# Optimization experiments

Measured on AMD Instinct MI355X. Metric: run time of the kernel, lower is better.

The kernel has to match this reference:

```python
import jax, jax.numpy as jnp
import numpy as np

D_MODEL = 512
N_HEADS = 8
MAX_CH = 128
LN_EPS = 1e-5


def setup_inputs() -> dict:
    key = jax.random.key(0)
    ks = jax.random.split(key, 8)
    B, T, C, D = 8, 256, 64, D_MODEL
    x = jax.random.normal(ks[0], (B, T, C, D), dtype=jnp.float32)
    # nn.MultiheadAttention params: packed in_proj [3D, D], out_proj [D, D]
    in_proj_w = jax.random.normal(ks[1], (3 * D, D), dtype=jnp.float32) * 0.02
    in_proj_b = jnp.zeros((3 * D,), dtype=jnp.float32)
    out_proj_w = jax.random.normal(ks[2], (D, D), dtype=jnp.float32) * 0.02
    out_proj_b = jnp.zeros((D,), dtype=jnp.float32)
    ln_g = jnp.ones((D,), dtype=jnp.float32)
    ln_b = jnp.zeros((D,), dtype=jnp.float32)
    rel_pos_bias = jax.random.normal(ks[3], (N_HEADS, MAX_CH, MAX_CH), dtype=jnp.float32) * 0.02
    return {"x": x, "in_proj_w": in_proj_w, "in_proj_b": in_proj_b,
            "out_proj_w": out_proj_w, "out_proj_b": out_proj_b,
            "ln_g": ln_g, "ln_b": ln_b, "rel_pos_bias": rel_pos_bias}


def _layernorm(x, g, b):
    mu = jnp.mean(x, axis=-1, keepdims=True)
    var = jnp.var(x, axis=-1, keepdims=True)
    return (x - mu) * jax.lax.rsqrt(var + LN_EPS) * g + b


def reference(x, in_proj_w, in_proj_b, out_proj_w, out_proj_b, ln_g, ln_b, rel_pos_bias):
    B, T, C, D = x.shape
    H = N_HEADS
    hd = D // H
    N = B * T
    xf = x.reshape(N, C, D)
    # 2D additive attn_mask: mean over heads of rel-pos bias, broadcast over heads/batch
    bias = jnp.mean(rel_pos_bias[:, :C, :C], axis=0)  # [C, C]
    qkv = xf @ in_proj_w.T + in_proj_b  # [N, C, 3D]
    q, k, v = jnp.split(qkv, 3, axis=-1)
    q = q.reshape(N, C, H, hd)
    k = k.reshape(N, C, H, hd)
    v = v.reshape(N, C, H, hd)
    scores = jnp.einsum('nqhd,nkhd->nhqk', q, k) / jnp.sqrt(jnp.float32(hd))
    scores = scores + bias[None, None, :, :]
    attn = jax.nn.softmax(scores, axis=-1)
    ctx = jnp.einsum('nhqk,nkhd->nqhd', attn, v).reshape(N, C, D)
    attn_out = ctx @ out_proj_w.T + out_proj_b
    out = _layernorm(xf + attn_out, ln_g, ln_b)
    return out.reshape(B, T, C, D)
```

## Files before the change

### kernel.cpp

```cpp
#include <hip/hip_runtime.h>
#include <stdint.h>
#include <stddef.h>


typedef __attribute__((ext_vector_type(8))) short short8;
typedef __attribute__((ext_vector_type(4))) float f32x4;

typedef __attribute__((address_space(3))) unsigned int as3_u32;
typedef __attribute__((address_space(1))) unsigned int as1_u32;

#define VMCNT5 asm volatile("s_waitcnt vmcnt(5)" ::: "memory")
#define VMCNT4 asm volatile("s_waitcnt vmcnt(4)" ::: "memory")
#define VMCNT0 asm volatile("s_waitcnt vmcnt(0)" ::: "memory")
#define LGKM0  asm volatile("s_waitcnt lgkmcnt(0)" ::: "memory")
#define BARR() __builtin_amdgcn_s_barrier()
#define PRIO1  __builtin_amdgcn_s_setprio(1)
#define PRIO0  __builtin_amdgcn_s_setprio(0)

__device__ __forceinline__ unsigned short f2bf(float f) {
  unsigned u = __builtin_bit_cast(unsigned, f);
  u = (u + 0x7FFFu + ((u >> 16) & 1u)) >> 16;
  return (unsigned short)u;
}

__device__ __forceinline__ f32x4 mfma16(short8 a, short8 b, f32x4 c) {
  return __builtin_amdgcn_mfma_f32_16x16x32_bf16(a, b, c, 0, 0, 0);
}

__device__ __forceinline__ short8 rd72(const char* buf, int row, int kelem) {
  return *(const short8*)(buf + row * 144 + kelem * 2);
}

__device__ __forceinline__ void stage16k(char* ldsbase, const char* gsrc, int w, int lane) {
#pragma unroll
  for (int j = 0; j < 4; ++j) {
    int off = j * 4096 + w * 1024;
    __builtin_amdgcn_global_load_lds((const as1_u32*)(gsrc + off + lane * 16),
                                     (as3_u32*)(ldsbase + off), 16, 0, 0);
  }
}

__global__ void prep_kernel(const float* __restrict__ wqkv_f,
                            const float* __restrict__ wo_f,
                            const float* __restrict__ rel,
                            unsigned short* __restrict__ wt,
                            float* __restrict__ bias2d) {
  int b = blockIdx.x, tid = threadIdx.x;
  if (b < 128) {
    unsigned short* dst = wt + (size_t)b * 8192;
#pragma unroll
    for (int t = 0; t < 4; ++t) {
      int u = t * 256 + tid;
      int row = u >> 4, us = u & 15;
      int kg = (us & 8) | ((us ^ row) & 7);
      const float* src;
      if (b < 96) {
        int h = b / 12, i = b % 12;
        int rg = i >> 2, kc = i & 3;
        src = wqkv_f + (size_t)(rg * 512 + h * 64 + row) * 512 + kc * 128 + kg * 8;
      } else {
        int cw = b - 96;
        int kc = cw >> 3, ng = cw & 7;
        src = wo_f + (size_t)(ng * 64 + row) * 512 + kc * 128 + kg * 8;
      }
      float4 a = *(const float4*)src;
      float4 c = *(const float4*)(src + 4);
      unsigned p0 = (unsigned)f2bf(a.x) | ((unsigned)f2bf(a.y) << 16);
      unsigned p1 = (unsigned)f2bf(a.z) | ((unsigned)f2bf(a.w) << 16);
      unsigned p2 = (unsigned)f2bf(c.x) | ((unsigned)f2bf(c.y) << 16);
      unsigned p3 = (unsigned)f2bf(c.z) | ((unsigned)f2bf(c.w) << 16);
      *(uint4*)(dst + u * 8) = make_uint4(p0, p1, p2, p3);
    }
  } else {
    int idx = (b - 128) * 256 + tid;
    int m = idx >> 6, nn = idx & 63;
    float s = 0.f;
#pragma unroll
    for (int hh = 0; hh < 8; ++hh) s += rel[hh * 16384 + m * 128 + nn];
    bias2d[idx] = s * 0.125f;
  }
}

__global__ __launch_bounds__(256, 2) void attn_qkv(
    const float* __restrict__ x,
    const char* __restrict__ wq,
    const float* __restrict__ bqkv,
    const float* __restrict__ bias2d,
    char* __restrict__ ctxg) {
  __shared__ __attribute__((aligned(16))) char smem[60416];
  char* B0 = smem;
  char* B1 = smem + 9216;
  char* B2 = smem + 18432;
  char* WSb = smem + 27648;

  const int n = blockIdx.x;
  const int tid = threadIdx.x;
  const int w = tid >> 6, lane = tid & 63;
  const int l15 = lane & 15, g = lane >> 4;
  const int wm = w >> 1, wn = w & 1;
  const int mrow = w * 16 + g * 4;
  const int wrow = w * 16 + l15;

  float b2d[16];
#pragma unroll
  for (int nt = 0; nt < 4; ++nt)
#pragma unroll
    for (int r = 0; r < 4; ++r)
      b2d[nt * 4 + r] = bias2d[(mrow + r) * 64 + nt * 16 + l15];

  stage16k(WSb, wq, w, lane);

  short8 xf[32];
#pragma unroll
  for (int mt = 0; mt < 2; ++mt) {
    const float* xr = x + ((size_t)n * 64 + wm * 32 + mt * 16 + l15) * 512;
#pragma unroll
    for (int kk = 0; kk < 16; ++kk) {
      float4 a = *(const float4*)(xr + kk * 32 + g * 8);
      float4 c = *(const float4*)(xr + kk * 32 + g * 8 + 4);
      short8 s;
      s[0] = (short)f2bf(a.x); s[1] = (short)f2bf(a.y);
      s[2] = (short)f2bf(a.z); s[3] = (short)f2bf(a.w);
      s[4] = (short)f2bf(c.x); s[5] = (short)f2bf(c.y);
      s[6] = (short)f2bf(c.z); s[7] = (short)f2bf(c.w);
      xf[mt * 16 + kk] = s;
    }
  }

  int b = 0;
  for (int h = 0; h < 8; ++h) {
    float bq2[2], bk2[2], bv2[2];
#pragma unroll
    for (int nt = 0; nt < 2; ++nt) {
      int col = h * 64 + wn * 32 + nt * 16 + l15;
      bq2[nt] = bqkv[col];
      bk2[nt] = bqkv[512 + col];
      bv2[nt] = bqkv[1024 + col];
    }
#pragma unroll
    for (int rg = 0; rg < 3; ++rg) {
      f32x4 acc[2][2] = {};
#pragma unroll
      for (int c = 0; c < 4; ++c) {
        if (b < 95)
          stage16k(WSb + (((b + 1) & 1) << 14), wq + (size_t)(b + 1) * 16384, w, lane);
        if (b < 95) { VMCNT4; } else { VMCNT0; }
        BARR();
        const char* ws = WSb + ((b & 1) << 14);
        PRIO1;
#pragma unroll
        for (int ks = 0; ks < 4; ++ks) {
#pragma unroll
          for (int nt = 0; nt < 2; ++nt) {
            int row = wn * 32 + nt * 16 + l15;
            int kg = ks * 4 + g;
            int us = (kg & 8) | ((kg ^ row) & 7);
            short8 bfr = *(const short8*)(ws + row * 256 + us * 16);
            acc[0][nt] = mfma16(xf[c * 4 + ks], bfr, acc[0][nt]);
            acc[1][nt] = mfma16(xf[16 + c * 4 + ks], bfr, acc[1][nt]);
          }
        }
        PRIO0;
        LGKM0; BARR();
        ++b;
      }
      if (rg == 0) {
#pragma unroll
        for (int mt = 0; mt < 2; ++mt)
#pragma unroll
          for (int nt = 0; nt < 2; ++nt)
#pragma unroll
            for (int r = 0; r < 4; ++r)
              *(unsigned short*)(B0 + (wm * 32 + mt * 16 + g * 4 + r) * 144 +
                                 (wn * 32 + nt * 16 + l15) * 2) =
                  f2bf(acc[mt][nt][r] + bq2[nt]);
      } else if (rg == 1) {
#pragma unroll
        for (int mt = 0; mt < 2; ++mt)
#pragma unroll
          for (int nt = 0; nt < 2; ++nt)
#pragma unroll
            for (int r = 0; r < 4; ++r)
              *(unsigned short*)(B1 + (wm * 32 + mt * 16 + g * 4 + r) * 144 +
                                 (wn * 32 + nt * 16 + l15) * 2) =
                  f2bf(acc[mt][nt][r] + bk2[nt]);
      } else {
#pragma unroll
        for (int mt = 0; mt < 2; ++mt)
#pragma unroll
          for (int nt = 0; nt < 2; ++nt) {
            unsigned short p0 = f2bf(acc[mt][nt][0] + bv2[nt]);
            unsigned short p1 = f2bf(acc[mt][nt][1] + bv2[nt]);
            unsigned short p2 = f2bf(acc[mt][nt][2] + bv2[nt]);
            unsigned short p3 = f2bf(acc[mt][nt][3] + bv2[nt]);
            unsigned lo = (unsigned)p0 | ((unsigned)p1 << 16);
            unsigned hi = (unsigned)p2 | ((unsigned)p3 << 16);
            *(uint2*)(B2 + (wn * 32 + nt * 16 + l15) * 144 +
                      (wm * 32 + mt * 16 + g * 4) * 2) = make_uint2(lo, hi);
          }
      }
    }
    LGKM0; BARR();

    {
      f32x4 sc[4] = {};
      short8 aq0 = rd72(B0, wrow, g * 8);
      short8 aq1 = rd72(B0, wrow, 32 + g * 8);
#pragma unroll
      for (int nt = 0; nt < 4; ++nt)
        sc[nt] = mfma16(aq0, rd72(B1, nt * 16 + l15, g * 8), sc[nt]);
#pragma unroll
      for (int nt = 0; nt < 4; ++nt)
        sc[nt] = mfma16(aq1, rd72(B1, nt * 16 + l15, 32 + g * 8), sc[nt]);
      float mx[4] = {-1e30f, -1e30f, -1e30f, -1e30f};
#pragma unroll
      for (int nt = 0; nt < 4; ++nt)
#pragma unroll
        for (int r = 0; r < 4; ++r) {
          float v = sc[nt][r] * 0.125f + b2d[nt * 4 + r];
          sc[nt][r] = v;
          mx[r] = fmaxf(mx[r], v);
        }
#pragma unroll
      for (int mk = 1; mk < 16; mk <<= 1)
#pragma unroll
        for (int r = 0; r < 4; ++r) mx[r] = fmaxf(mx[r], __shfl_xor(mx[r], mk));
      float sm[4] = {0.f, 0.f, 0.f, 0.f};
#pragma unroll
      for (int nt = 0; nt < 4; ++nt)
#pragma unroll
        for (int r = 0; r < 4; ++r) {
          float e = __expf(sc[nt][r] - mx[r]);
          sc[nt][r] = e;
          sm[r] += e;
        }
#pragma unroll
      for (int mk = 1; mk < 16; mk <<= 1)
#pragma unroll
        for (int r = 0; r < 4; ++r) sm[r] += __shfl_xor(sm[r], mk);
      float inv[4];
#pragma unroll
      for (int r = 0; r < 4; ++r) inv[r] = 1.0f / sm[r];
#pragma unroll
      for (int nt = 0; nt < 4; ++nt)
#pragma unroll
        for (int r = 0; r < 4; ++r)
          *(unsigned short*)(B0 + (mrow + r) * 144 + (nt * 16 + l15) * 2) =
              f2bf(sc[nt][r] * inv[r]);
    }

    f32x4 cv[4] = {};
    {
      short8 ap0 = rd72(B0, wrow, g * 8);
      short8 ap1 = rd72(B0, wrow, 32 + g * 8);
#pragma unroll
      for (int nt = 0; nt < 4; ++nt)
        cv[nt] = mfma16(ap0, rd72(B2, nt * 16 + l15, g * 8), cv[nt]);
#pragma unroll
      for (int nt = 0; nt < 4; ++nt)
        cv[nt] = mfma16(ap1, rd72(B2, nt * 16 + l15, 32 + g * 8), cv[nt]);
    }
    LGKM0; BARR();
#pragma unroll
    for (int nt = 0; nt < 4; ++nt)
#pragma unroll
      for (int r = 0; r < 4; ++r)
        *(unsigned short*)(B2 + (mrow + r) * 144 + (nt * 16 + l15) * 2) =
            f2bf(cv[nt][r]);
    LGKM0; BARR();

    {
      char* cdst = ctxg + (size_t)n * 131072 + (h >> 1) * 16384 + (h & 1) * 128;
#pragma unroll
      for (int it = 0; it < 2; ++it) {
        int flat = it * 256 + tid;
        int row = flat >> 3, uu = flat & 7;
        uint4 v = *(const uint4*)(B2 + row * 144 + uu * 16);
        int slot = uu ^ (row & 7);
        *(uint4*)(cdst + row * 256 + slot * 16) = v;
      }
    }
  }
}

__global__ __launch_bounds__(256, 2) void oproj_ln(
    const char* __restrict__ ctxg,
    const char* __restrict__ wo,
    const float* __restrict__ bo,
    const float* __restrict__ x,
    const float* __restrict__ lng,
    const float* __restrict__ lnb,
    float* __restrict__ out) {
  __shared__ __attribute__((aligned(16))) char smem[65536];
  char* WB = smem;
  char* CB = smem + 32768;
  float* EP  = (float*)smem;
  float* SM1 = (float*)(smem + 32768);
  float* SM2 = (float*)(smem + 33408);

  const int n = blockIdx.x;
  const int tid = threadIdx.x;
  const int w = tid >> 6, lane = tid & 63;
  const int l15 = lane & 15, g = lane >> 4;
  const int um = w >> 1, un = w & 1;

  const char* cbase = ctxg + (size_t)n * 131072;

  stage16k(CB, cbase, w, lane);
  stage16k(WB, wo, w, lane);

  f32x4 acc[8][2][2] = {};

  for (int kc = 0; kc < 4; ++kc) {
    short8 actx[2][4];
#pragma unroll
    for (int ng = 0; ng < 8; ++ng) {
      int b = kc * 8 + ng;
      if (b < 31)
        stage16k(WB + (((b + 1) & 1) << 14), wo + (size_t)(b + 1) * 16384, w, lane);
      if ((ng & 1) == 0 && kc < 3) {
        int p = ng >> 1;
        int off = p * 4096 + w * 1024;
        __builtin_amdgcn_global_load_lds(
            (const as1_u32*)(cbase + (kc + 1) * 16384 + off + lane * 16),
            (as3_u32*)(CB + (((kc + 1) & 1) << 14) + off), 16, 0, 0);
      }
      if (b < 31) { VMCNT5; } else { VMCNT0; }
      BARR();
      const char* cb = CB + ((kc & 1) << 14);
      if (ng == 0) {
#pragma unroll
        for (int mt = 0; mt < 2; ++mt)
#pragma unroll
          for (int ks = 0; ks < 4; ++ks) {
            int row = um * 32 + mt * 16 + l15;
            int u = ks * 4 + g;
            int us = u ^ (row & 7);
            actx[mt][ks] = *(const short8*)(cb + row * 256 + us * 16);
          }
      }
      const char* ws = WB + ((b & 1) << 14);
      PRIO1;
#pragma unroll
      for (int ks = 0; ks < 4; ++ks) {
#pragma unroll
        for (int nt = 0; nt < 2; ++nt) {
          int row = un * 32 + nt * 16 + l15;
          int kg = ks * 4 + g;
          int us = (kg & 8) | ((kg ^ row) & 7);
          short8 bfr = *(const short8*)(ws + row * 256 + us * 16);
          acc[ng][0][nt] = mfma16(actx[0][ks], bfr, acc[ng][0][nt]);
          acc[ng][1][nt] = mfma16(actx[1][ks], bfr, acc[ng][1][nt]);
        }
      }
      PRIO0;
      LGKM0; BARR();
    }
  }

  VMCNT0;
  const float* xblk = x + (size_t)n * 32768;
  float* oblk = out + (size_t)n * 32768;
  float s1[2][4] = {}, s2[2][4] = {};

#pragma unroll
  for (int ng = 0; ng < 8; ++ng) {
#pragma unroll
    for (int t = 0; t < 4; ++t) {
      int flat = t * 256 + tid;
      int row = flat >> 4, f4 = flat & 15;
      float4 v = *(const float4*)(xblk + row * 512 + ng * 64 + f4 * 4);
      *(float4*)(EP + row * 68 + f4 * 4) = v;
    }
    LGKM0; BARR();
    float boA[2];
#pragma unroll
    for (int nt = 0; nt < 2; ++nt) boA[nt] = bo[ng * 64 + un * 32 + nt * 16 + l15];
#pragma unroll
    for (int mt = 0; mt < 2; ++mt)
#pragma unroll
      for (int nt = 0; nt < 2; ++nt)
#pragma unroll
        for (int r = 0; r < 4; ++r) {
          int row = um * 32 + mt * 16 + g * 4 + r;
          float xv = EP[row * 68 + un * 32 + nt * 16 + l15];
          float v = acc[ng][mt][nt][r] + boA[nt] + xv;
          acc[ng][mt][nt][r] = v;
          s1[mt][r] += v;
          s2[mt][r] += v * v;
        }
    LGKM0; BARR();
  }
#pragma unroll
  for (int mk = 1; mk < 16; mk <<= 1)
#pragma unroll
    for (int mt = 0; mt < 2; ++mt)
#pragma unroll
      for (int r = 0; r < 4; ++r) {
        s1[mt][r] += __shfl_xor(s1[mt][r], mk);
        s2[mt][r] += __shfl_xor(s2[mt][r], mk);
      }
  if (l15 == 0) {
#pragma unroll
    for (int mt = 0; mt < 2; ++mt)
#pragma unroll
      for (int r = 0; r < 4; ++r) {
        int row = um * 32 + mt * 16 + g * 4 + r;
        SM1[row * 2 + un] = s1[mt][r];
        SM2[row * 2 + un] = s2[mt][r];
      }
  }
  LGKM0; BARR();
  float mu[2][4], rs[2][4];
#pragma unroll
  for (int mt = 0; mt < 2; ++mt)
#pragma unroll
    for (int r = 0; r < 4; ++r) {
      int row = um * 32 + mt * 16 + g * 4 + r;
      float a1 = SM1[row * 2] + SM1[row * 2 + 1];
      float a2 = SM2[row * 2] + SM2[row * 2 + 1];
      float m = a1 * (1.0f / 512.0f);
      float var = a2 * (1.0f / 512.0f) - m * m;
      mu[mt][r] = m;
      rs[mt][r] = rsqrtf(var + 1e-5f);
    }
  BARR();
#pragma unroll
  for (int ng = 0; ng < 8; ++ng) {
    float lgA[2], lbA[2];
#pragma unroll
    for (int nt = 0; nt < 2; ++nt) {
      int col = ng * 64 + un * 32 + nt * 16 + l15;
      lgA[nt] = lng[col];
      lbA[nt] = lnb[col];
    }
#pragma unroll
    for (int mt = 0; mt < 2; ++mt)
#pragma unroll
      for (int nt = 0; nt < 2; ++nt)
#pragma unroll
        for (int r = 0; r < 4; ++r) {
          int row = um * 32 + mt * 16 + g * 4 + r;
          EP[row * 68 + un * 32 + nt * 16 + l15] =
              (acc[ng][mt][nt][r] - mu[mt][r]) * rs[mt][r] * lgA[nt] + lbA[nt];
        }
    LGKM0; BARR();
#pragma unroll
    for (int t = 0; t < 4; ++t) {
      int flat = t * 256 + tid;
      int row = flat >> 4, f4 = flat & 15;
      *(float4*)(oblk + row * 512 + ng * 64 + f4 * 4) =
          *(const float4*)(EP + row * 68 + f4 * 4);
    }
    BARR();
  }
}

extern "C" void kernel_launch(void* const* d_in, const int* in_sizes, int n_in,
                              void* d_out, int out_size, void* d_ws, size_t ws_size,
                              hipStream_t stream) {
  const float* x    = (const float*)d_in[0];
  const float* wqkv = (const float*)d_in[1];
  const float* bqkv = (const float*)d_in[2];
  const float* wo   = (const float*)d_in[3];
  const float* bo   = (const float*)d_in[4];
  const float* lng  = (const float*)d_in[5];
  const float* lnb  = (const float*)d_in[6];
  const float* rel  = (const float*)d_in[7];

  unsigned short* wt = (unsigned short*)d_ws;
  float* bias2d = (float*)((char*)d_ws + 128 * 16384);
  const char* wqc = (const char*)d_ws;
  const char* woc = (const char*)d_ws + 96 * 16384;

  prep_kernel<<<144, 256, 0, stream>>>(wqkv, wo, rel, wt, bias2d);
  attn_qkv<<<2048, 256, 0, stream>>>(x, wqc, bqkv, bias2d, (char*)d_out);
  oproj_ln<<<2048, 256, 0, stream>>>((const char*)d_out, woc, bo, x, lng, lnb,
                                     (float*)d_out);
}
```

Baseline: 578.2 us.

## Triple-buffer QKV weight staging and switch attention tiles to XOR-swizzled layout

```diff
diff --git a/kernel.cpp b/kernel.cpp
--- a/kernel.cpp
+++ b/kernel.cpp
@@ -9,6 +9,7 @@
 typedef __attribute__((address_space(3))) unsigned int as3_u32;
 typedef __attribute__((address_space(1))) unsigned int as1_u32;
 
+#define VMCNT8 asm volatile("s_waitcnt vmcnt(8)" ::: "memory")
 #define VMCNT5 asm volatile("s_waitcnt vmcnt(5)" ::: "memory")
 #define VMCNT4 asm volatile("s_waitcnt vmcnt(4)" ::: "memory")
 #define VMCNT0 asm volatile("s_waitcnt vmcnt(0)" ::: "memory")
@@ -27,8 +28,16 @@
   return __builtin_amdgcn_mfma_f32_16x16x32_bf16(a, b, c, 0, 0, 0);
 }
 
-__device__ __forceinline__ short8 rd72(const char* buf, int row, int kelem) {
-  return *(const short8*)(buf + row * 144 + kelem * 2);
+__device__ __forceinline__ short8 rd8s(const char* buf, int row, int unit) {
+  return *(const short8*)(buf + row * 128 + ((unit ^ (row & 7)) * 16));
+}
+__device__ __forceinline__ void wr2s(char* buf, int row, int col, unsigned short v) {
+  int slot = (col >> 3) ^ (row & 7);
+  *(unsigned short*)(buf + row * 128 + slot * 16 + (col & 7) * 2) = v;
+}
+__device__ __forceinline__ void wr8s(char* buf, int row, int col, uint2 v) {
+  int slot = (col >> 3) ^ (row & 7);
+  *(uint2*)(buf + row * 128 + slot * 16 + (col & 7) * 2) = v;
 }
 
 __device__ __forceinline__ void stage16k(char* ldsbase, const char* gsrc, int w, int lane) {
@@ -87,11 +96,11 @@
     const float* __restrict__ bqkv,
     const float* __restrict__ bias2d,
     char* __restrict__ ctxg) {
-  __shared__ __attribute__((aligned(16))) char smem[60416];
-  char* B0 = smem;
-  char* B1 = smem + 9216;
-  char* B2 = smem + 18432;
-  char* WSb = smem + 27648;
+  extern __shared__ __attribute__((aligned(16))) char smem[];
+  char* WS = smem;
+  char* B0 = smem + 49152;
+  char* B1 = smem + 57344;
+  char* B2 = smem + 65536;
 
   const int n = blockIdx.x;
   const int tid = threadIdx.x;
@@ -100,15 +109,6 @@
   const int wm = w >> 1, wn = w & 1;
   const int mrow = w * 16 + g * 4;
   const int wrow = w * 16 + l15;
-
-  float b2d[16];
-#pragma unroll
-  for (int nt = 0; nt < 4; ++nt)
-#pragma unroll
-    for (int r = 0; r < 4; ++r)
-      b2d[nt * 4 + r] = bias2d[(mrow + r) * 64 + nt * 16 + l15];
-
-  stage16k(WSb, wq, w, lane);
 
   short8 xf[32];
 #pragma unroll
@@ -126,8 +126,17 @@
       xf[mt * 16 + kk] = s;
     }
   }
-
-  int b = 0;
+  float b2d[16];
+#pragma unroll
+  for (int nt = 0; nt < 4; ++nt)
+#pragma unroll
+    for (int r = 0; r < 4; ++r)
+      b2d[nt * 4 + r] = bias2d[(mrow + r) * 64 + nt * 16 + l15];
+
+  stage16k(WS, wq, w, lane);
+  stage16k(WS + 16384, wq + 16384, w, lane);
+
+  int b = 0, cur = 0;
   for (int h = 0; h < 8; ++h) {
     float bq2[2], bk2[2], bv2[2];
 #pragma unroll
@@ -142,11 +151,13 @@
       f32x4 acc[2][2] = {};
 #pragma unroll
       for (int c = 0; c < 4; ++c) {
-        if (b < 95)
-          stage16k(WSb + (((b + 1) & 1) << 14), wq + (size_t)(b + 1) * 16384, w, lane);
-        if (b < 95) { VMCNT4; } else { VMCNT0; }
+        int tgt = cur + 2; if (tgt >= 3) tgt -= 3;
+        if (b + 2 < 96) {
+          stage16k(WS + tgt * 16384, wq + (size_t)(b + 2) * 16384, w, lane);
+          VMCNT8;
+        } else if (b + 1 < 96) { VMCNT4; } else { VMCNT0; }
         BARR();
-        const char* ws = WSb + ((b & 1) << 14);
+        const char* ws = WS + cur * 16384;
         PRIO1;
 #pragma unroll
         for (int ks = 0; ks < 4; ++ks) {
@@ -162,7 +173,7 @@
         }
         PRIO0;
         LGKM0; BARR();
-        ++b;
+        ++b; ++cur; if (cur >= 3) cur -= 3;
       }
       if (rg == 0) {
 #pragma unroll
@@ -171,9 +182,8 @@
           for (int nt = 0; nt < 2; ++nt)
 #pragma unroll
             for (int r = 0; r < 4; ++r)
-              *(unsigned short*)(B0 + (wm * 32 + mt * 16 + g * 4 + r) * 144 +
-                                 (wn * 32 + nt * 16 + l15) * 2) =
-                  f2bf(acc[mt][nt][r] + bq2[nt]);
+              wr2s(B0, wm * 32 + mt * 16 + g * 4 + r, wn * 32 + nt * 16 + l15,
+                   f2bf(acc[mt][nt][r] + bq2[nt]));
       } else if (rg == 1) {
 #pragma unroll
         for (int mt = 0; mt < 2; ++mt)
@@ -181,9 +191,8 @@
           for (int nt = 0; nt < 2; ++nt)
 #pragma unroll
             for (int r = 0; r < 4; ++r)
-              *(unsigned short*)(B1 + (wm * 32 + mt * 16 + g * 4 + r) * 144 +
-                                 (wn * 32 + nt * 16 + l15) * 2) =
-                  f2bf(acc[mt][nt][r] + bk2[nt]);
+              wr2s(B1, wm * 32 + mt * 16 + g * 4 + r, wn * 32 + nt * 16 + l15,
+                   f2bf(acc[mt][nt][r] + bk2[nt]));
       } else {
 #pragma unroll
         for (int mt = 0; mt < 2; ++mt)
@@ -195,8 +204,8 @@
             unsigned short p3 = f2bf(acc[mt][nt][3] + bv2[nt]);
             unsigned lo = (unsigned)p0 | ((unsigned)p1 << 16);
             unsigned hi = (unsigned)p2 | ((unsigned)p3 << 16);
-            *(uint2*)(B2 + (wn * 32 + nt * 16 + l15) * 144 +
-                      (wm * 32 + mt * 16 + g * 4) * 2) = make_uint2(lo, hi);
+            wr8s(B2, wn * 32 + nt * 16 + l15, wm * 32 + mt * 16 + g * 4,
+                 make_uint2(lo, hi));
           }
       }
     }
@@ -204,14 +213,14 @@
 
     {
       f32x4 sc[4] = {};
-      short8 aq0 = rd72(B0, wrow, g * 8);
-      short8 aq1 = rd72(B0, wrow, 32 + g * 8);
-#pragma unroll
-      for (int nt = 0; nt < 4; ++nt)
-        sc[nt] = mfma16(aq0, rd72(B1, nt * 16 + l15, g * 8), sc[nt]);
-#pragma unroll
-      for (int nt = 0; nt < 4; ++nt)
-        sc[nt] = mfma16(aq1, rd72(B1, nt * 16 + l15, 32 + g * 8), sc[nt]);
+      short8 aq0 = rd8s(B0, wrow, g);
+      short8 aq1 = rd8s(B0, wrow, 4 + g);
+#pragma unroll
+      for (int nt = 0; nt < 4; ++nt)
+        sc[nt] = mfma16(aq0, rd8s(B1, nt * 16 + l15, g), sc[nt]);
+#pragma unroll
+      for (int nt = 0; nt < 4; ++nt)
+        sc[nt] = mfma16(aq1, rd8s(B1, nt * 16 + l15, 4 + g), sc[nt]);
       float mx[4] = {-1e30f, -1e30f, -1e30f, -1e30f};
 #pragma unroll
       for (int nt = 0; nt < 4; ++nt)
@@ -245,39 +254,36 @@
       for (int nt = 0; nt < 4; ++nt)
 #pragma unroll
         for (int r = 0; r < 4; ++r)
-          *(unsigned short*)(B0 + (mrow + r) * 144 + (nt * 16 + l15) * 2) =
-              f2bf(sc[nt][r] * inv[r]);
+          wr2s(B0, mrow + r, nt * 16 + l15, f2bf(sc[nt][r] * inv[r]));
     }
 
     f32x4 cv[4] = {};
     {
-      short8 ap0 = rd72(B0, wrow, g * 8);
-      short8 ap1 = rd72(B0, wrow, 32 + g * 8);
-#pragma unroll
-      for (int nt = 0; nt < 4; ++nt)
-        cv[nt] = mfma16(ap0, rd72(B2, nt * 16 + l15, g * 8), cv[nt]);
-#pragma unroll
-      for (int nt = 0; nt < 4; ++nt)
-        cv[nt] = mfma16(ap1, rd72(B2, nt * 16 + l15, 32 + g * 8), cv[nt]);
-    }
+      short8 ap0 = rd8s(B0, wrow, g);
+      short8 ap1 = rd8s(B0, wrow, 4 + g);
+#pragma unroll
+      for (int nt = 0; nt < 4; ++nt)
+        cv[nt] = mfma16(ap0, rd8s(B2, nt * 16 + l15, g), cv[nt]);
+#pragma unroll
+      for (int nt = 0; nt < 4; ++nt)
+        cv[nt] = mfma16(ap1, rd8s(B2, nt * 16 + l15, 4 + g), cv[nt]);
+    }
+    BARR();
+#pragma unroll
+    for (int nt = 0; nt < 4; ++nt)
+#pragma unroll
+      for (int r = 0; r < 4; ++r)
+        wr2s(B1, mrow + r, nt * 16 + l15, f2bf(cv[nt][r]));
     LGKM0; BARR();
-#pragma unroll
-    for (int nt = 0; nt < 4; ++nt)
-#pragma unroll
-      for (int r = 0; r < 4; ++r)
-        *(unsigned short*)(B2 + (mrow + r) * 144 + (nt * 16 + l15) * 2) =
-            f2bf(cv[nt][r]);
-    LGKM0; BARR();
 
     {
-      char* cdst = ctxg + (size_t)n * 131072 + (h >> 1) * 16384 + (h & 1) * 128;
+      char* cdst = ctxg + (size_t)n * 131072 + h * 8192;
 #pragma unroll
       for (int it = 0; it < 2; ++it) {
         int flat = it * 256 + tid;
-        int row = flat >> 3, uu = flat & 7;
-        uint4 v = *(const uint4*)(B2 + row * 144 + uu * 16);
-        int slot = uu ^ (row & 7);
-        *(uint4*)(cdst + row * 256 + slot * 16) = v;
+        int row = flat >> 3, s = flat & 7;
+        uint4 v = *(const uint4*)(B1 + row * 128 + s * 16);
+        *(uint4*)(cdst + row * 128 + s * 16) = v;
       }
     }
   }
@@ -335,8 +341,8 @@
           for (int ks = 0; ks < 4; ++ks) {
             int row = um * 32 + mt * 16 + l15;
             int u = ks * 4 + g;
-            int us = u ^ (row & 7);
-            actx[mt][ks] = *(const short8*)(cb + row * 256 + us * 16);
+            actx[mt][ks] = *(const short8*)(cb + (u >> 3) * 8192 + row * 128 +
+                                            (((u & 7) ^ (row & 7)) * 16));
           }
       }
       const char* ws = WB + ((b & 1) << 14);
@@ -473,8 +479,11 @@
   const char* wqc = (const char*)d_ws;
   const char* woc = (const char*)d_ws + 96 * 16384;
 
+  hipFuncSetAttribute(reinterpret_cast<const void*>(attn_qkv),
+                      hipFuncAttributeMaxDynamicSharedMemorySize, 73728);
+
   prep_kernel<<<144, 256, 0, stream>>>(wqkv, wo, rel, wt, bias2d);
-  attn_qkv<<<2048, 256, 0, stream>>>(x, wqc, bqkv, bias2d, (char*)d_out);
+  attn_qkv<<<2048, 256, 73728, stream>>>(x, wqc, bqkv, bias2d, (char*)d_out);
   oproj_ln<<<2048, 256, 0, stream>>>((const char*)d_out, woc, bo, x, lng, lnb,
                                      (float*)d_out);
 }
```

Result: faster. 548.2 us (-5.2%).
